# Kernel tuning notes

Measured on AMD Instinct MI355X. Metric: run time of the kernel, lower is better.

Reference implementation:

```python
import jax, jax.numpy as jnp
import numpy as np

EPS_TERN = 1e-8


def _ternarize(w):
    # scale = mean(|w|) + 1e-8; quantize to {-1, 0, 1}
    scale = jnp.abs(w).mean() + EPS_TERN
    return jnp.clip(jnp.round(w / scale), -1.0, 1.0)


def _rmsnorm(x):
    # torch nn.RMSNorm with elementwise_affine=False, eps=None -> finfo(dtype).eps
    eps = jnp.finfo(x.dtype).eps
    ms = jnp.mean(x * x, axis=-1, keepdims=True)
    return x * jax.lax.rsqrt(ms + eps)


def _block(x, w):
    # RMSNorm -> SiLU -> ternary linear (F.linear: x @ w.T)
    h = jax.nn.silu(_rmsnorm(x))
    return h @ _ternarize(w).T


def setup_inputs() -> dict:
    key = jax.random.key(0)
    k0, k1, k2, k3 = jax.random.split(key, 4)
    d = 4096
    n_tok = 8192
    # kaiming_normal_ for [out, in]: std = sqrt(2 / fan_in)
    std = np.sqrt(2.0 / d).astype(np.float32)
    return {
        "x": jax.random.normal(k0, (n_tok, d), dtype=jnp.float32),
        "w0": jax.random.normal(k1, (d, d), dtype=jnp.float32) * std,
        "w1": jax.random.normal(k2, (d, d), dtype=jnp.float32) * std,
        "w2": jax.random.normal(k3, (d, d), dtype=jnp.float32) * std,
    }


def reference(x, w0, w1, w2):
    for w in (w0, w1, w2):
        x = _block(x, w)
    return x
```

## Files before the change

### kernel.cpp

```cpp
#include <hip/hip_runtime.h>
#include <stdint.h>

typedef unsigned short u16;
typedef __attribute__((ext_vector_type(8))) __bf16 bf16x8;
typedef __attribute__((ext_vector_type(8))) short short8;
typedef __attribute__((ext_vector_type(4))) float f32x4;

#define D_DIM 4096
#define M_TOK 8192
#define BM 128
#define BN 128
#define BK 64

__device__ __forceinline__ u16 f2bf(float f) {
  unsigned u = __builtin_bit_cast(unsigned, f);
  u += 0x7fffu + ((u >> 16) & 1u);
  return (u16)(u >> 16);
}
__device__ __forceinline__ float bf2f(u16 b) {
  unsigned u = ((unsigned)b) << 16;
  return __builtin_bit_cast(float, u);
}

#define LOAD_LDS16(gp, lp)                                                     \
  __builtin_amdgcn_global_load_lds(                                            \
      (const __attribute__((address_space(1))) void*)((const void*)(gp)),      \
      (__attribute__((address_space(3))) void*)((void*)(lp)), 16, 0, 0)

__global__ void abs_partial_k(const float* __restrict__ w, float* __restrict__ partial) {
  const int n4 = (D_DIM * D_DIM) / 4;
  float s = 0.f;
  for (int i = blockIdx.x * 256 + threadIdx.x; i < n4; i += 1024 * 256) {
    float4 v = ((const float4*)w)[i];
    s += fabsf(v.x) + fabsf(v.y) + fabsf(v.z) + fabsf(v.w);
  }
#pragma unroll
  for (int o = 32; o > 0; o >>= 1) s += __shfl_down(s, o, 64);
  __shared__ float sm[4];
  if ((threadIdx.x & 63) == 0) sm[threadIdx.x >> 6] = s;
  __syncthreads();
  if (threadIdx.x == 0) partial[blockIdx.x] = sm[0] + sm[1] + sm[2] + sm[3];
}

__global__ void finalize_scale_k(const float* __restrict__ partial, float* __restrict__ scale) {
  float s = 0.f;
  for (int i = threadIdx.x; i < 1024; i += 256) s += partial[i];
#pragma unroll
  for (int o = 32; o > 0; o >>= 1) s += __shfl_down(s, o, 64);
  __shared__ float sm[4];
  if ((threadIdx.x & 63) == 0) sm[threadIdx.x >> 6] = s;
  __syncthreads();
  if (threadIdx.x == 0)
    scale[0] = (sm[0] + sm[1] + sm[2] + sm[3]) * (1.0f / 16777216.0f) + 1e-8f;
}

__global__ void ternarize_k(const float* __restrict__ w, u16* __restrict__ t,
                            const float* __restrict__ scale) {
  const float sc = scale[0];
  int i = blockIdx.x * 256 + threadIdx.x;
  float4 v = ((const float4*)w)[i];
  ushort4 o;
  o.x = f2bf(fminf(fmaxf(rintf(v.x / sc), -1.f), 1.f));
  o.y = f2bf(fminf(fmaxf(rintf(v.y / sc), -1.f), 1.f));
  o.z = f2bf(fminf(fmaxf(rintf(v.z / sc), -1.f), 1.f));
  o.w = f2bf(fminf(fmaxf(rintf(v.w / sc), -1.f), 1.f));
  ((ushort4*)t)[i] = o;
}

__global__ void rms_silu_f32_k(const float* __restrict__ x, u16* __restrict__ h) {
  const int row = blockIdx.x;
  const float4* xr = (const float4*)(x + (size_t)row * D_DIM);
  float4 v[4];
  float ss = 0.f;
#pragma unroll
  for (int i = 0; i < 4; ++i) {
    v[i] = xr[threadIdx.x + i * 256];
    ss += v[i].x * v[i].x + v[i].y * v[i].y + v[i].z * v[i].z + v[i].w * v[i].w;
  }
#pragma unroll
  for (int o = 32; o > 0; o >>= 1) ss += __shfl_down(ss, o, 64);
  __shared__ float sm[4];
  if ((threadIdx.x & 63) == 0) sm[threadIdx.x >> 6] = ss;
  __syncthreads();
  const float ms = (sm[0] + sm[1] + sm[2] + sm[3]) * (1.0f / (float)D_DIM);
  const float r = rsqrtf(ms + 1.1920929e-7f);
  ushort4* hr = (ushort4*)(h + (size_t)row * D_DIM);
#pragma unroll
  for (int i = 0; i < 4; ++i) {
    float z0 = v[i].x * r, z1 = v[i].y * r, z2 = v[i].z * r, z3 = v[i].w * r;
    ushort4 o;
    o.x = f2bf(z0 / (1.f + __expf(-z0)));
    o.y = f2bf(z1 / (1.f + __expf(-z1)));
    o.z = f2bf(z2 / (1.f + __expf(-z2)));
    o.w = f2bf(z3 / (1.f + __expf(-z3)));
    hr[threadIdx.x + i * 256] = o;
  }
}

__global__ void rms_silu_bf16_k(const u16* __restrict__ x, u16* __restrict__ h) {
  const int row = blockIdx.x;
  const ushort4* xr = (const ushort4*)(x + (size_t)row * D_DIM);
  float4 v[4];
  float ss = 0.f;
#pragma unroll
  for (int i = 0; i < 4; ++i) {
    ushort4 b = xr[threadIdx.x + i * 256];
    v[i] = make_float4(bf2f(b.x), bf2f(b.y), bf2f(b.z), bf2f(b.w));
    ss += v[i].x * v[i].x + v[i].y * v[i].y + v[i].z * v[i].z + v[i].w * v[i].w;
  }
#pragma unroll
  for (int o = 32; o > 0; o >>= 1) ss += __shfl_down(ss, o, 64);
  __shared__ float sm[4];
  if ((threadIdx.x & 63) == 0) sm[threadIdx.x >> 6] = ss;
  __syncthreads();
  const float ms = (sm[0] + sm[1] + sm[2] + sm[3]) * (1.0f / (float)D_DIM);
  const float r = rsqrtf(ms + 1.1920929e-7f);
  ushort4* hr = (ushort4*)(h + (size_t)row * D_DIM);
#pragma unroll
  for (int i = 0; i < 4; ++i) {
    float z0 = v[i].x * r, z1 = v[i].y * r, z2 = v[i].z * r, z3 = v[i].w * r;
    ushort4 o;
    o.x = f2bf(z0 / (1.f + __expf(-z0)));
    o.y = f2bf(z1 / (1.f + __expf(-z1)));
    o.z = f2bf(z2 / (1.f + __expf(-z2)));
    o.w = f2bf(z3 / (1.f + __expf(-z3)));
    hr[threadIdx.x + i * 256] = o;
  }
}

template <typename OUT>
__global__ __launch_bounds__(256) void gemm_bt_k(
    const u16* __restrict__ A, const u16* __restrict__ B, OUT* __restrict__ C,
    int M, int N, int K) {
  __shared__ u16 As[BM * BK];
  __shared__ u16 Bs[BN * BK];

  const int tid = threadIdx.x;
  const int wave = tid >> 6;
  const int lane = tid & 63;

  const int bm = blockIdx.x * BM;
  const int bn = blockIdx.y * BN;
  const int wm = (wave >> 1) * 64;
  const int wn = (wave & 1) * 64;

  const int fr = lane & 15;
  const int fq = lane >> 4;
  const int m3 = fr & 7;
  const int aoff0 = (wm + fr) * BK + ((fq ^ m3) << 3);
  const int aoff1 = (wm + fr) * BK + (((4 + fq) ^ m3) << 3);
  const int boff0 = (wn + fr) * BK + ((fq ^ m3) << 3);
  const int boff1 = (wn + fr) * BK + (((4 + fq) ^ m3) << 3);

  const int srow = lane >> 3;
  const int sblk = (lane & 7) ^ srow;
  const size_t ldK = (size_t)K;
  const u16* agp = A + (size_t)(bm + wave * 32 + srow) * ldK + (size_t)(sblk * 8);
  const u16* bgp = B + (size_t)(bn + wave * 32 + srow) * ldK + (size_t)(sblk * 8);
  u16* asd = &As[wave * 2048];
  u16* bsd = &Bs[wave * 2048];

  f32x4 acc[4][4];
#pragma unroll
  for (int i = 0; i < 4; ++i)
#pragma unroll
    for (int j = 0; j < 4; ++j) acc[i][j] = {0.f, 0.f, 0.f, 0.f};

  for (int k0 = 0; k0 < K; k0 += BK) {
    __syncthreads();
#pragma unroll
    for (int i = 0; i < 4; ++i) {
      LOAD_LDS16(agp + (size_t)(i * 8) * ldK, asd + i * 512);
      LOAD_LDS16(bgp + (size_t)(i * 8) * ldK, bsd + i * 512);
    }
    agp += BK;
    bgp += BK;
    __syncthreads();

#pragma unroll
    for (int kk = 0; kk < 2; ++kk) {
      const int ao = kk ? aoff1 : aoff0;
      const int bo = kk ? boff1 : boff0;
      bf16x8 af[4], bfr[4];
#pragma unroll
      for (int mi = 0; mi < 4; ++mi)
        af[mi] = __builtin_bit_cast(bf16x8, *(const short8*)&As[ao + mi * (16 * BK)]);
#pragma unroll
      for (int ni = 0; ni < 4; ++ni)
        bfr[ni] = __builtin_bit_cast(bf16x8, *(const short8*)&Bs[bo + ni * (16 * BK)]);
#pragma unroll
      for (int mi = 0; mi < 4; ++mi)
#pragma unroll
        for (int ni = 0; ni < 4; ++ni)
          acc[mi][ni] = __builtin_amdgcn_mfma_f32_16x16x32_bf16(
              af[mi], bfr[ni], acc[mi][ni], 0, 0, 0);
    }
  }

  const int crow0 = bm + wm + (lane >> 4) * 4;
  const int ccol0 = bn + wn + (lane & 15);
#pragma unroll
  for (int mi = 0; mi < 4; ++mi)
#pragma unroll
    for (int ni = 0; ni < 4; ++ni)
#pragma unroll
      for (int r = 0; r < 4; ++r) {
        float v = acc[mi][ni][r];
        size_t idx = (size_t)(crow0 + mi * 16 + r) * N + (ccol0 + ni * 16);
        if constexpr (__is_same(OUT, float))
          C[idx] = v;
        else
          C[idx] = f2bf(v);
      }
}

extern "C" void kernel_launch(void* const* d_in, const int* in_sizes, int n_in,
                              void* d_out, int out_size, void* d_ws, size_t ws_size,
                              hipStream_t stream) {
  const float* x = (const float*)d_in[0];
  const float* w[3] = {(const float*)d_in[1], (const float*)d_in[2], (const float*)d_in[3]};

  char* ws = (char*)d_ws;
  float* scale = (float*)ws;
  float* partial = (float*)(ws + 256);
  u16* tW = (u16*)(ws + 8192);
  u16* h = (u16*)(ws + 8192 + 33554432);
  u16* xmid = (u16*)(ws + 8192 + 33554432 + 67108864);

  dim3 grid(M_TOK / BM, D_DIM / BN);
  for (int l = 0; l < 3; ++l) {
    abs_partial_k<<<1024, 256, 0, stream>>>(w[l], partial);
    finalize_scale_k<<<1, 256, 0, stream>>>(partial, scale);
    ternarize_k<<<(D_DIM * D_DIM) / 4 / 256, 256, 0, stream>>>(w[l], tW, scale);
    if (l == 0)
      rms_silu_f32_k<<<M_TOK, 256, 0, stream>>>(x, h);
    else
      rms_silu_bf16_k<<<M_TOK, 256, 0, stream>>>(xmid, h);
    if (l == 2)
      gemm_bt_k<float><<<grid, 256, 0, stream>>>(h, tW, (float*)d_out, M_TOK, D_DIM, D_DIM);
    else
      gemm_bt_k<u16><<<grid, 256, 0, stream>>>(h, tW, xmid, M_TOK, D_DIM, D_DIM);
  }
}
```

Before: 1.369 ms.

## Rewrite GEMM with 256x256 tiles, 4-stage LDS ring pipeline, XCD-aware tile mapping

Replaces the single-buffered 128x128x64 GEMM, which synchronizes twice per k-step, with a 512-thread 256x256 tile kernel. It uses a 4-slot LDS ring of BK=32 slices, prefetches two stages ahead, and syncs once per step with a vmcnt wait plus barrier. Blocks are remapped to spread tiles across the 8 XCDs, and MFMA issue is given raised priority. This aims to hide global-load latency, raise arithmetic intensity per tile and improve L2 locality. In exchange it uses 8x4 accumulators per wave, which raises register pressure under launch_bounds(512,2).

```diff
diff --git a/kernel.cpp b/kernel.cpp
--- a/kernel.cpp
+++ b/kernel.cpp
@@ -8,9 +8,11 @@
 
 #define D_DIM 4096
 #define M_TOK 8192
-#define BM 128
-#define BN 128
-#define BK 64
+
+#define BM 256
+#define BN 256
+#define BKS 32
+#define SLICE_U16 (BM * BKS)
 
 __device__ __forceinline__ u16 f2bf(float f) {
   unsigned u = __builtin_bit_cast(unsigned, f);
@@ -129,78 +131,97 @@
 }
 
 template <typename OUT>
-__global__ __launch_bounds__(256) void gemm_bt_k(
+__global__ __launch_bounds__(512, 2) void gemm_bt_k(
     const u16* __restrict__ A, const u16* __restrict__ B, OUT* __restrict__ C,
     int M, int N, int K) {
-  __shared__ u16 As[BM * BK];
-  __shared__ u16 Bs[BN * BK];
+  __shared__ u16 As[4][SLICE_U16];
+  __shared__ u16 Bs[4][SLICE_U16];
 
   const int tid = threadIdx.x;
   const int wave = tid >> 6;
   const int lane = tid & 63;
 
-  const int bm = blockIdx.x * BM;
-  const int bn = blockIdx.y * BN;
-  const int wm = (wave >> 1) * 64;
-  const int wn = (wave & 1) * 64;
+  const int nwg = gridDim.x;
+  const int cpx = nwg >> 3;
+  const int bid = blockIdx.x;
+  const int lid = (bid & 7) * cpx + (bid >> 3);
+  const int tilesM = M >> 8;
+  const int tm = lid % tilesM;
+  const int tn = lid / tilesM;
+  const int bm = tm * BM;
+  const int bn = tn * BN;
+
+  const int wr = wave >> 2;
+  const int wc = wave & 3;
+  const int wm = wr * 128;
+  const int wn = wc * 64;
 
   const int fr = lane & 15;
   const int fq = lane >> 4;
-  const int m3 = fr & 7;
-  const int aoff0 = (wm + fr) * BK + ((fq ^ m3) << 3);
-  const int aoff1 = (wm + fr) * BK + (((4 + fq) ^ m3) << 3);
-  const int boff0 = (wn + fr) * BK + ((fq ^ m3) << 3);
-  const int boff1 = (wn + fr) * BK + (((4 + fq) ^ m3) << 3);
-
-  const int srow = lane >> 3;
-  const int sblk = (lane & 7) ^ srow;
+  const int g = fq ^ ((fr >> 2) & 3);
+  const int aoff = (wm + fr) * BKS + g * 8;
+  const int boff = (wn + fr) * BKS + g * 8;
+
+  const int srow = lane >> 2;
+  const int sg = (lane & 3) ^ ((lane >> 4) & 3);
   const size_t ldK = (size_t)K;
-  const u16* agp = A + (size_t)(bm + wave * 32 + srow) * ldK + (size_t)(sblk * 8);
-  const u16* bgp = B + (size_t)(bn + wave * 32 + srow) * ldK + (size_t)(sblk * 8);
-  u16* asd = &As[wave * 2048];
-  u16* bsd = &Bs[wave * 2048];
-
-  f32x4 acc[4][4];
-#pragma unroll
-  for (int i = 0; i < 4; ++i)
+  const u16* agp = A + (size_t)(bm + wave * 16 + srow) * ldK + (size_t)(sg * 8);
+  const u16* bgp = B + (size_t)(bn + wave * 16 + srow) * ldK + (size_t)(sg * 8);
+  const int sdst = wave * 16 * BKS;
+
+  f32x4 acc[8][4];
+#pragma unroll
+  for (int i = 0; i < 8; ++i)
 #pragma unroll
     for (int j = 0; j < 4; ++j) acc[i][j] = {0.f, 0.f, 0.f, 0.f};
 
-  for (int k0 = 0; k0 < K; k0 += BK) {
-    __syncthreads();
-#pragma unroll
-    for (int i = 0; i < 4; ++i) {
-      LOAD_LDS16(agp + (size_t)(i * 8) * ldK, asd + i * 512);
-      LOAD_LDS16(bgp + (size_t)(i * 8) * ldK, bsd + i * 512);
-    }
-    agp += BK;
-    bgp += BK;
-    __syncthreads();
-
-#pragma unroll
-    for (int kk = 0; kk < 2; ++kk) {
-      const int ao = kk ? aoff1 : aoff0;
-      const int bo = kk ? boff1 : boff0;
-      bf16x8 af[4], bfr[4];
-#pragma unroll
-      for (int mi = 0; mi < 4; ++mi)
-        af[mi] = __builtin_bit_cast(bf16x8, *(const short8*)&As[ao + mi * (16 * BK)]);
-#pragma unroll
-      for (int ni = 0; ni < 4; ++ni)
-        bfr[ni] = __builtin_bit_cast(bf16x8, *(const short8*)&Bs[bo + ni * (16 * BK)]);
-#pragma unroll
-      for (int mi = 0; mi < 4; ++mi)
-#pragma unroll
-        for (int ni = 0; ni < 4; ++ni)
-          acc[mi][ni] = __builtin_amdgcn_mfma_f32_16x16x32_bf16(
-              af[mi], bfr[ni], acc[mi][ni], 0, 0, 0);
-    }
-  }
+#define STAGE(s, r)                                                            \
+  do {                                                                         \
+    const u16* a0 = agp + (size_t)(s)*BKS;                                     \
+    const u16* b0 = bgp + (size_t)(s)*BKS;                                     \
+    LOAD_LDS16(a0, &As[r][sdst]);                                              \
+    LOAD_LDS16(a0 + (size_t)128 * ldK, &As[r][sdst + 128 * BKS]);              \
+    LOAD_LDS16(b0, &Bs[r][sdst]);                                              \
+    LOAD_LDS16(b0 + (size_t)128 * ldK, &Bs[r][sdst + 128 * BKS]);              \
+  } while (0)
+
+#define COMPUTE(r)                                                             \
+  do {                                                                         \
+    const u16* ab = &As[r][aoff];                                              \
+    const u16* bb = &Bs[r][boff];                                              \
+    bf16x8 bfv[4];                                                             \
+    _Pragma("unroll") for (int ni = 0; ni < 4; ++ni) bfv[ni] =                 \
+        __builtin_bit_cast(bf16x8, *(const short8*)(bb + ni * (16 * BKS)));    \
+    __builtin_amdgcn_s_setprio(1);                                             \
+    _Pragma("unroll") for (int mi = 0; mi < 8; ++mi) {                         \
+      bf16x8 af =                                                              \
+          __builtin_bit_cast(bf16x8, *(const short8*)(ab + mi * (16 * BKS))); \
+      _Pragma("unroll") for (int ni = 0; ni < 4; ++ni) acc[mi][ni] =           \
+          __builtin_amdgcn_mfma_f32_16x16x32_bf16(af, bfv[ni],                 \
+                                                  acc[mi][ni], 0, 0, 0);       \
+    }                                                                          \
+    __builtin_amdgcn_s_setprio(0);                                             \
+  } while (0)
+
+  const int ns = K / BKS;
+  STAGE(0, 0);
+  STAGE(1, 1);
+  asm volatile("s_waitcnt vmcnt(4)\n\ts_barrier" ::: "memory");
+  for (int s = 0; s < ns - 2; ++s) {
+    STAGE(s + 2, (s + 2) & 3);
+    COMPUTE(s & 3);
+    asm volatile("s_waitcnt vmcnt(4)\n\ts_barrier" ::: "memory");
+  }
+  COMPUTE((ns - 2) & 3);
+  asm volatile("s_waitcnt vmcnt(0)\n\ts_barrier" ::: "memory");
+  COMPUTE((ns - 1) & 3);
+#undef STAGE
+#undef COMPUTE
 
   const int crow0 = bm + wm + (lane >> 4) * 4;
   const int ccol0 = bn + wn + (lane & 15);
 #pragma unroll
-  for (int mi = 0; mi < 4; ++mi)
+  for (int mi = 0; mi < 8; ++mi)
 #pragma unroll
     for (int ni = 0; ni < 4; ++ni)
 #pragma unroll
@@ -227,7 +248,7 @@
   u16* h = (u16*)(ws + 8192 + 33554432);
   u16* xmid = (u16*)(ws + 8192 + 33554432 + 67108864);
 
-  dim3 grid(M_TOK / BM, D_DIM / BN);
+  dim3 grid((M_TOK / BM) * (D_DIM / BN));
   for (int l = 0; l < 3; ++l) {
     abs_partial_k<<<1024, 256, 0, stream>>>(w[l], partial);
     finalize_scale_k<<<1, 256, 0, stream>>>(partial, scale);
@@ -237,8 +258,8 @@
     else
       rms_silu_bf16_k<<<M_TOK, 256, 0, stream>>>(xmid, h);
     if (l == 2)
-      gemm_bt_k<float><<<grid, 256, 0, stream>>>(h, tW, (float*)d_out, M_TOK, D_DIM, D_DIM);
+      gemm_bt_k<float><<<grid, 512, 0, stream>>>(h, tW, (float*)d_out, M_TOK, D_DIM, D_DIM);
     else
-      gemm_bt_k<u16><<<grid, 256, 0, stream>>>(h, tW, xmid, M_TOK, D_DIM, D_DIM);
-  }
-}
+      gemm_bt_k<u16><<<grid, 512, 0, stream>>>(h, tW, xmid, M_TOK, D_DIM, D_DIM);
+  }
+}
```

New measurement: 1.484 ms. 1.08x slower.
